# Kernel tuning notes

Hardware: AMD Instinct MI355X
Metric: run time of the kernel (lower is better)

The kernel has to match this reference:

```python
import jax, jax.numpy as jnp
import numpy as np
import math

B, S, D, H = 4, 2048, 768, 12
DK = D // H

def setup_inputs() -> dict:
    key = jax.random.key(0)
    ks = jax.random.split(key, 12)
    sc = 1.0 / math.sqrt(D)
    return {
        'Q': jax.random.normal(ks[0], (B, S, D), jnp.float32),
        'K': jax.random.normal(ks[1], (B, S, D), jnp.float32),
        'V': jax.random.normal(ks[2], (B, S, D), jnp.float32),
        'mask': jax.random.randint(ks[3], (B, 1, S, S), 0, 2, jnp.int32),
        'Wq': jax.random.normal(ks[4], (D, D), jnp.float32) * sc,
        'bq': jnp.zeros((D,), jnp.float32),
        'Wk': jax.random.normal(ks[5], (D, D), jnp.float32) * sc,
        'bk': jnp.zeros((D,), jnp.float32),
        'Wv': jax.random.normal(ks[6], (D, D), jnp.float32) * sc,
        'bv': jnp.zeros((D,), jnp.float32),
        'Wo': jax.random.normal(ks[7], (D, D), jnp.float32) * sc,
        'bo': jnp.zeros((D,), jnp.float32),
    }

def _split_heads(x):
    # [B,S,D] -> [B,H,S,DK]
    return x.reshape(B, S, H, DK).transpose(0, 2, 1, 3)

def reference(Q, K, V, mask, Wq, bq, Wk, bk, Wv, bv, Wo, bo):
    q = _split_heads(Q @ Wq.T + bq)
    k = _split_heads(K @ Wk.T + bk)
    v = _split_heads(V @ Wv.T + bv)
    scores = jnp.einsum('bhqd,bhkd->bhqk', q, k) / math.sqrt(DK)
    # Faithful to the source: masked positions are filled with -1e-9 (NOT -inf)
    scores = jnp.where(mask == 0, jnp.float32(-1e-9), scores)
    attn = jax.nn.softmax(scores, axis=-1)
    x = jnp.einsum('bhqk,bhkd->bhqd', attn, v)          # [B,H,S,DK]
    x = x.transpose(0, 2, 1, 3).reshape(B, S, D)         # [B,S,D]
    return x @ Wo.T + bo
```

## Files before the change

### kernel.cpp

```cpp
#include <hip/hip_runtime.h>

#define BB 4
#define SS 2048
#define DD 768
#define HH 12
#define DKK 64
#define MM (BB*SS)

typedef __attribute__((ext_vector_type(8))) short bf16x8;
typedef __attribute__((ext_vector_type(4))) float f32x4;

#define GLDS(g, l) __builtin_amdgcn_global_load_lds( \
    (const __attribute__((address_space(1))) unsigned int*)(g), \
    (__attribute__((address_space(3))) unsigned int*)(l), 16, 0, 0)

__device__ __forceinline__ unsigned short f2bf(float f) {
    union { float f; unsigned int u; } v; v.f = f;
    unsigned int r = v.u + 0x7fffu + ((v.u >> 16) & 1u);
    return (unsigned short)(r >> 16);
}

#define NACT4 (MM*DD/4)
#define ABLK  (NACT4/256)
#define NW4   (DD*DD/4)
#define WBLK  (NW4/256)
#define MBLK  (BB*SS*SS/256)

__global__ void prep(
    const float* __restrict__ Q, const float* __restrict__ K, const float* __restrict__ V,
    const float* __restrict__ Wq, const float* __restrict__ Wk, const float* __restrict__ Wv,
    const float* __restrict__ Wo, const int* __restrict__ mask,
    unsigned short* __restrict__ Qc, unsigned short* __restrict__ Kc, unsigned short* __restrict__ Vc,
    unsigned short* __restrict__ Wqc, unsigned short* __restrict__ Wkc, unsigned short* __restrict__ Wvc,
    unsigned short* __restrict__ Woc, unsigned int* __restrict__ mbits)
{
    const int bx = blockIdx.x;
    if (bx < 3 * ABLK) {
        const int seg = bx / ABLK;
        const float* s = seg == 0 ? Q : seg == 1 ? K : V;
        unsigned short* d = seg == 0 ? Qc : seg == 1 ? Kc : Vc;
        const int i = (bx - seg * ABLK) * 256 + threadIdx.x;
        float4 v = ((const float4*)s)[i];
        ushort4 o;
        o.x = f2bf(v.x); o.y = f2bf(v.y); o.z = f2bf(v.z); o.w = f2bf(v.w);
        ((ushort4*)d)[i] = o;
    } else if (bx < 3 * ABLK + 4 * WBLK) {
        const int b2 = bx - 3 * ABLK;
        const int seg = b2 / WBLK;
        const float* s = seg == 0 ? Wq : seg == 1 ? Wk : seg == 2 ? Wv : Wo;
        unsigned short* d = seg == 0 ? Wqc : seg == 1 ? Wkc : seg == 2 ? Wvc : Woc;
        const int i = (b2 - seg * WBLK) * 256 + threadIdx.x;
        float4 v = ((const float4*)s)[i];
        ushort4 o;
        o.x = f2bf(v.x); o.y = f2bf(v.y); o.z = f2bf(v.z); o.w = f2bf(v.w);
        ((ushort4*)d)[i] = o;
    } else {
        const int t = (bx - (3 * ABLK + 4 * WBLK)) * 256 + threadIdx.x;
        const int m = mask[t];
        unsigned long long b = __ballot(m != 0);
        const int l = t & 63;
        if (l == 0)       mbits[t >> 5] = (unsigned int)b;
        else if (l == 32) mbits[t >> 5] = (unsigned int)(b >> 32);
    }
}

__global__ __launch_bounds__(256) void gemm_qkv(
    const unsigned short* __restrict__ Qc, const unsigned short* __restrict__ Kc, const unsigned short* __restrict__ Vc,
    const unsigned short* __restrict__ Wq, const unsigned short* __restrict__ Wk, const unsigned short* __restrict__ Wv,
    const float* __restrict__ bq, const float* __restrict__ bk, const float* __restrict__ bv,
    unsigned short* __restrict__ qb, unsigned short* __restrict__ kb, unsigned short* __restrict__ vt)
{
    __shared__ unsigned short As[128*32];
    __shared__ unsigned short Bs[128*32];
    const int mat = blockIdx.z;
    const unsigned short* X = mat == 0 ? Qc : mat == 1 ? Kc : Vc;
    const unsigned short* W = mat == 0 ? Wq : mat == 1 ? Wk : Wv;
    const float* bias        = mat == 0 ? bq : mat == 1 ? bk : bv;

    const int tid  = threadIdx.x;
    const int lane = tid & 63;
    const int w    = tid >> 6;
    const int wm   = w >> 1, wn = w & 1;
    const int quad = lane >> 4, c = lane & 15;
    const int m0 = blockIdx.y * 128, n0 = blockIdx.x * 128;

    f32x4 acc[4][4];
    #pragma unroll
    for (int i = 0; i < 4; i++)
        #pragma unroll
        for (int j = 0; j < 4; j++) acc[i][j] = (f32x4){0.f, 0.f, 0.f, 0.f};

    const int ch0 = tid, ch1 = 256 + tid;
    const int r0 = ch0 >> 2, cc0 = (ch0 & 3) << 3;
    const int r1 = ch1 >> 2, cc1 = (ch1 & 3) << 3;
    const unsigned short* Xg0 = X + (size_t)(m0 + r0) * DD + cc0;
    const unsigned short* Xg1 = X + (size_t)(m0 + r1) * DD + cc1;
    const unsigned short* Wg0 = W + (size_t)(n0 + r0) * DD + cc0;
    const unsigned short* Wg1 = W + (size_t)(n0 + r1) * DD + cc1;

    for (int k0 = 0; k0 < DD; k0 += 32) {
        GLDS(Xg0 + k0, As + ch0 * 8);
        GLDS(Xg1 + k0, As + ch1 * 8);
        GLDS(Wg0 + k0, Bs + ch0 * 8);
        GLDS(Wg1 + k0, Bs + ch1 * 8);
        __syncthreads();
        bf16x8 a[4], b[4];
        #pragma unroll
        for (int t = 0; t < 4; t++) {
            a[t] = *(const bf16x8*)(As + ((wm * 64 + t * 16 + c) * 32 + quad * 8));
            b[t] = *(const bf16x8*)(Bs + ((wn * 64 + t * 16 + c) * 32 + quad * 8));
        }
        #pragma unroll
        for (int tm = 0; tm < 4; tm++)
            #pragma unroll
            for (int tn = 0; tn < 4; tn++)
                acc[tm][tn] = __builtin_amdgcn_mfma_f32_16x16x32_bf16(a[tm], b[tn], acc[tm][tn], 0, 0, 0);
        __syncthreads();
    }

    if (mat < 2) {
        unsigned short* out = mat == 0 ? qb : kb;
        #pragma unroll
        for (int tn = 0; tn < 4; tn++) {
            const int col = n0 + wn * 64 + tn * 16 + c;
            const float bz = bias[col];
            #pragma unroll
            for (int tm = 0; tm < 4; tm++) {
                const int row = m0 + wm * 64 + tm * 16 + quad * 4;
                #pragma unroll
                for (int r = 0; r < 4; r++)
                    out[(size_t)(row + r) * DD + col] = f2bf(acc[tm][tn][r] + bz);
            }
        }
    } else {
        #pragma unroll
        for (int tn = 0; tn < 4; tn++) {
            const int col = n0 + wn * 64 + tn * 16 + c;
            const float bz = bias[col];
            const int h = col >> 6, dk = col & 63;
            #pragma unroll
            for (int tm = 0; tm < 4; tm++) {
                const int row = m0 + wm * 64 + tm * 16 + quad * 4;
                const int bb = row >> 11, s = row & 2047;
                ushort4 pk;
                pk.x = f2bf(acc[tm][tn][0] + bz);
                pk.y = f2bf(acc[tm][tn][1] + bz);
                pk.z = f2bf(acc[tm][tn][2] + bz);
                pk.w = f2bf(acc[tm][tn][3] + bz);
                *(ushort4*)(vt + ((((size_t)bb * HH + h) * DKK + dk) * SS + s)) = pk;
            }
        }
    }
}

#define EXPSCALE 0.18033688011112042f

__global__ __launch_bounds__(256, 3) void flash(
    const unsigned short* __restrict__ qb, const unsigned short* __restrict__ kb,
    const unsigned short* __restrict__ vt, const unsigned int* __restrict__ mbits,
    unsigned short* __restrict__ ob)
{
    __shared__ unsigned short Ks[2][64*64];
    __shared__ unsigned short Vs[2][64*64];

    const int bh = blockIdx.y;
    const int bi = bh / HH, h = bh % HH;
    const int tid  = threadIdx.x;
    const int w    = tid >> 6, lane = tid & 63;
    const int quad = lane >> 4, c = lane & 15;
    const int q0w = blockIdx.x * 128 + w * 32;

    bf16x8 qa[2][2];
    #pragma unroll
    for (int mt = 0; mt < 2; mt++) {
        const unsigned short* qbase = qb + (size_t)(bi * SS + q0w + mt * 16 + c) * DD + h * DKK + quad * 8;
        qa[mt][0] = *(const bf16x8*)(qbase);
        qa[mt][1] = *(const bf16x8*)(qbase + 32);
    }

    const int l0 = tid >> 3, sl = tid & 7;
    const int l1 = 32 + l0;
    const int lc = (sl ^ (l0 & 7)) << 3;
    const int kp0 = ((l0 >> 5) << 5) | (((l0 >> 2) & 3) << 3) | (((l0 >> 4) & 1) << 2) | (l0 & 3);
    const int kp1 = ((l1 >> 5) << 5) | (((l1 >> 2) & 3) << 3) | (((l1 >> 4) & 1) << 2) | (l1 & 3);
    const unsigned short* kg0 = kb + ((size_t)bi * SS + kp0) * DD + h * DKK + lc;
    const unsigned short* kg1 = kb + ((size_t)bi * SS + kp1) * DD + h * DKK + lc;
    const unsigned short* vg0 = vt + (((size_t)bi * HH + h) * DKK + l0) * SS + lc;
    const unsigned short* vg1 = vt + (((size_t)bi * HH + h) * DKK + l1) * SS + lc;

    const unsigned int* mrow0 = mbits + (size_t)(bi * SS + q0w + c) * (SS / 32);
    const unsigned int* mrow1 = mrow0 + (size_t)16 * (SS / 32);

    f32x4 o[2][4];
    #pragma unroll
    for (int mt = 0; mt < 2; mt++)
        #pragma unroll
        for (int dt = 0; dt < 4; dt++) o[mt][dt] = (f32x4){0.f, 0.f, 0.f, 0.f};
    float rs[2] = {0.f, 0.f};

    const int cswz = c & 7;

    GLDS(kg0, Ks[0] + (size_t)tid * 8);
    GLDS(kg1, Ks[0] + (size_t)(256 + tid) * 8);
    GLDS(vg0, Vs[0] + (size_t)tid * 8);
    GLDS(vg1, Vs[0] + (size_t)(256 + tid) * 8);

    for (int t = 0; t < SS / 64; t++) {
        const int k0 = t * 64, par = t & 1;
        __syncthreads();
        if (t < SS / 64 - 1) {
            const size_t ko = (size_t)(k0 + 64);
            GLDS(kg0 + ko * DD, Ks[par ^ 1] + (size_t)tid * 8);
            GLDS(kg1 + ko * DD, Ks[par ^ 1] + (size_t)(256 + tid) * 8);
            GLDS(vg0 + ko,      Vs[par ^ 1] + (size_t)tid * 8);
            GLDS(vg1 + ko,      Vs[par ^ 1] + (size_t)(256 + tid) * 8);
        }

        const uint2 mw0 = *(const uint2*)(mrow0 + (k0 >> 5));
        const uint2 mw1 = *(const uint2*)(mrow1 + (k0 >> 5));
        const unsigned long long mmq[2] = {
            ((((unsigned long long)mw0.y << 32) | mw0.x) >> (quad * 8)),
            ((((unsigned long long)mw1.y << 32) | mw1.x) >> (quad * 8)) };

        #pragma unroll
        for (int p = 0; p < 2; p++) {
            unsigned int pq[2][4];
            #pragma unroll
            for (int tt = 0; tt < 2; tt++) {
                const unsigned short* kbase = &Ks[par][((2 * p + tt) * 16 + c) << 6];
                const bf16x8 kf0 = *(const bf16x8*)(kbase + ((quad ^ cswz) << 3));
                const bf16x8 kf1 = *(const bf16x8*)(kbase + (((4 + quad) ^ cswz) << 3));
                #pragma unroll
                for (int mt = 0; mt < 2; mt++) {
                    f32x4 st = (f32x4){0.f, 0.f, 0.f, 0.f};
                    st = __builtin_amdgcn_mfma_f32_16x16x32_bf16(kf0, qa[mt][0], st, 0, 0, 0);
                    st = __builtin_amdgcn_mfma_f32_16x16x32_bf16(kf1, qa[mt][1], st, 0, 0, 0);
                    const unsigned int mb = (unsigned int)(mmq[mt] >> (p * 32 + tt * 4)) & 15u;
                    #pragma unroll
                    for (int r2 = 0; r2 < 2; r2++) {
                        float sv0 = st[r2 * 2]     * EXPSCALE;
                        float sv1 = st[r2 * 2 + 1] * EXPSCALE;
                        sv0 = (mb & (1u << (r2 * 2)))     ? sv0 : 0.0f;
                        sv1 = (mb & (1u << (r2 * 2 + 1))) ? sv1 : 0.0f;
                        const float p0 = __builtin_amdgcn_exp2f(sv0);
                        const float p1 = __builtin_amdgcn_exp2f(sv1);
                        rs[mt] += p0 + p1;
                        union { float f; unsigned int u; } u0, u1; u0.f = p0; u1.f = p1;
                        pq[mt][tt * 2 + r2] = __builtin_amdgcn_perm(u1.u + 0x8000u, u0.u + 0x8000u, 0x07060302);
                    }
                }
            }
            #pragma unroll
            for (int dt = 0; dt < 4; dt++) {
                const bf16x8 vf = *(const bf16x8*)(&Vs[par][((dt * 16 + c) << 6) + ((((p << 2) + quad) ^ cswz) << 3)]);
                #pragma unroll
                for (int mt = 0; mt < 2; mt++) {
                    union { unsigned int u[4]; bf16x8 v; } pb;
                    pb.u[0] = pq[mt][0]; pb.u[1] = pq[mt][1];
                    pb.u[2] = pq[mt][2]; pb.u[3] = pq[mt][3];
                    o[mt][dt] = __builtin_amdgcn_mfma_f32_16x16x32_bf16(vf, pb.v, o[mt][dt], 0, 0, 0);
                }
            }
        }
    }

    #pragma unroll
    for (int mt = 0; mt < 2; mt++) {
        float v = rs[mt];
        v += __shfl_xor(v, 16);
        v += __shfl_xor(v, 32);
        const float rn = __builtin_amdgcn_rcpf(v);
        unsigned short* op = ob + (size_t)(bi * SS + q0w + mt * 16 + c) * DD + h * DKK + quad * 4;
        #pragma unroll
        for (int dt = 0; dt < 4; dt++) {
            ushort4 pk;
            pk.x = f2bf(o[mt][dt][0] * rn);
            pk.y = f2bf(o[mt][dt][1] * rn);
            pk.z = f2bf(o[mt][dt][2] * rn);
            pk.w = f2bf(o[mt][dt][3] * rn);
            *(ushort4*)(op + dt * 16) = pk;
        }
    }
}

__global__ __launch_bounds__(256) void gemm_out(
    const unsigned short* __restrict__ A, const unsigned short* __restrict__ W,
    const float* __restrict__ bias, float* __restrict__ out)
{
    __shared__ unsigned short As[128*32];
    __shared__ unsigned short Bs[128*32];
    const int tid  = threadIdx.x;
    const int lane = tid & 63;
    const int w    = tid >> 6;
    const int wm   = w >> 1, wn = w & 1;
    const int quad = lane >> 4, c = lane & 15;
    const int m0 = blockIdx.y * 128, n0 = blockIdx.x * 128;

    f32x4 acc[4][4];
    #pragma unroll
    for (int i = 0; i < 4; i++)
        #pragma unroll
        for (int j = 0; j < 4; j++) acc[i][j] = (f32x4){0.f, 0.f, 0.f, 0.f};

    const int ch0 = tid, ch1 = 256 + tid;
    const int r0 = ch0 >> 2, cc0 = (ch0 & 3) << 3;
    const int r1 = ch1 >> 2, cc1 = (ch1 & 3) << 3;
    const unsigned short* Ag0 = A + (size_t)(m0 + r0) * DD + cc0;
    const unsigned short* Ag1 = A + (size_t)(m0 + r1) * DD + cc1;
    const unsigned short* Wg0 = W + (size_t)(n0 + r0) * DD + cc0;
    const unsigned short* Wg1 = W + (size_t)(n0 + r1) * DD + cc1;

    for (int k0 = 0; k0 < DD; k0 += 32) {
        GLDS(Ag0 + k0, As + ch0 * 8);
        GLDS(Ag1 + k0, As + ch1 * 8);
        GLDS(Wg0 + k0, Bs + ch0 * 8);
        GLDS(Wg1 + k0, Bs + ch1 * 8);
        __syncthreads();
        bf16x8 a[4], b[4];
        #pragma unroll
        for (int t = 0; t < 4; t++) {
            a[t] = *(const bf16x8*)(As + ((wm * 64 + t * 16 + c) * 32 + quad * 8));
            b[t] = *(const bf16x8*)(Bs + ((wn * 64 + t * 16 + c) * 32 + quad * 8));
        }
        #pragma unroll
        for (int tm = 0; tm < 4; tm++)
            #pragma unroll
            for (int tn = 0; tn < 4; tn++)
                acc[tm][tn] = __builtin_amdgcn_mfma_f32_16x16x32_bf16(a[tm], b[tn], acc[tm][tn], 0, 0, 0);
        __syncthreads();
    }

    #pragma unroll
    for (int tn = 0; tn < 4; tn++) {
        const int col = n0 + wn * 64 + tn * 16 + c;
        const float bz = bias[col];
        #pragma unroll
        for (int tm = 0; tm < 4; tm++) {
            const int row = m0 + wm * 64 + tm * 16 + quad * 4;
            #pragma unroll
            for (int r = 0; r < 4; r++)
                out[(size_t)(row + r) * DD + col] = acc[tm][tn][r] + bz;
        }
    }
}

extern "C" void kernel_launch(void* const* d_in, const int* in_sizes, int n_in,
                              void* d_out, int out_size, void* d_ws, size_t ws_size,
                              hipStream_t stream) {
    (void)in_sizes; (void)n_in; (void)out_size; (void)ws_size;
    const float* Q    = (const float*)d_in[0];
    const float* K    = (const float*)d_in[1];
    const float* V    = (const float*)d_in[2];
    const int*   mask = (const int*)d_in[3];
    const float* Wq   = (const float*)d_in[4];
    const float* bq   = (const float*)d_in[5];
    const float* Wk   = (const float*)d_in[6];
    const float* bk   = (const float*)d_in[7];
    const float* Wv   = (const float*)d_in[8];
    const float* bv   = (const float*)d_in[9];
    const float* Wo   = (const float*)d_in[10];
    const float* bo   = (const float*)d_in[11];
    float* out = (float*)d_out;

    char* ws = (char*)d_ws;
    size_t off = 0;
    auto alloc = [&](size_t bytes) { char* p = ws + off; off += (bytes + 255) & ~255ULL; return p; };
    const size_t act = (size_t)MM * DD * 2;
    unsigned short* Qc  = (unsigned short*)alloc(act);
    unsigned short* Kc  = (unsigned short*)alloc(act);
    unsigned short* Vc  = (unsigned short*)alloc(act);
    unsigned short* Wqc = (unsigned short*)alloc((size_t)DD * DD * 2);
    unsigned short* Wkc = (unsigned short*)alloc((size_t)DD * DD * 2);
    unsigned short* Wvc = (unsigned short*)alloc((size_t)DD * DD * 2);
    unsigned short* Woc = (unsigned short*)alloc((size_t)DD * DD * 2);
    unsigned short* qb  = (unsigned short*)alloc(act);
    unsigned short* kb  = (unsigned short*)alloc(act);
    unsigned short* vt  = (unsigned short*)alloc(act);
    unsigned int*  mbits = (unsigned int*)alloc((size_t)BB * SS * (SS / 32) * 4);
    unsigned short* ob = Qc;

    prep<<<dim3(3 * ABLK + 4 * WBLK + MBLK), 256, 0, stream>>>(
        Q, K, V, Wq, Wk, Wv, Wo, mask, Qc, Kc, Vc, Wqc, Wkc, Wvc, Woc, mbits);
    gemm_qkv<<<dim3(DD / 128, MM / 128, 3), 256, 0, stream>>>(
        Qc, Kc, Vc, Wqc, Wkc, Wvc, bq, bk, bv, qb, kb, vt);
    flash<<<dim3(SS / 128, BB * HH), 256, 0, stream>>>(qb, kb, vt, mbits, ob);
    gemm_out<<<dim3(DD / 128, MM / 128), 256, 0, stream>>>(ob, Woc, bo, out);
}
```

Baseline: 376.4 us.

## Widen GEMM K-tiles with swizzled LDS, fold softmax scale into Q, MFMA row sums

Both projection GEMMs now stage 64-wide K tiles with an XOR-swizzled LDS layout, which halves the number of barrier rounds and avoids bank conflicts. The exp2 scale factor is folded into the Q projection epilogue, removing a multiply per score in the flash kernel. The flash kernel computes row sums with an extra MFMA against a ones vector instead of scalar adds and cross-lane shuffles, and it prefetches mask words one tile ahead. The costs are doubled LDS use in the GEMMs, extra MFMA work per tile, and row sums taken from bf16-rounded probabilities.

```diff
diff --git a/kernel.cpp b/kernel.cpp
--- a/kernel.cpp
+++ b/kernel.cpp
@@ -19,6 +19,8 @@
     unsigned int r = v.u + 0x7fffu + ((v.u >> 16) & 1u);
     return (unsigned short)(r >> 16);
 }
+
+#define EXPSCALE 0.18033688011112042f
 
 #define NACT4 (MM*DD/4)
 #define ABLK  (NACT4/256)
@@ -70,8 +72,8 @@
     const float* __restrict__ bq, const float* __restrict__ bk, const float* __restrict__ bv,
     unsigned short* __restrict__ qb, unsigned short* __restrict__ kb, unsigned short* __restrict__ vt)
 {
-    __shared__ unsigned short As[128*32];
-    __shared__ unsigned short Bs[128*32];
+    __shared__ unsigned short As[128*64];
+    __shared__ unsigned short Bs[128*64];
     const int mat = blockIdx.z;
     const unsigned short* X = mat == 0 ? Qc : mat == 1 ? Kc : Vc;
     const unsigned short* W = mat == 0 ? Wq : mat == 1 ? Wk : Wv;
@@ -90,36 +92,47 @@
         #pragma unroll
         for (int j = 0; j < 4; j++) acc[i][j] = (f32x4){0.f, 0.f, 0.f, 0.f};
 
-    const int ch0 = tid, ch1 = 256 + tid;
-    const int r0 = ch0 >> 2, cc0 = (ch0 & 3) << 3;
-    const int r1 = ch1 >> 2, cc1 = (ch1 & 3) << 3;
-    const unsigned short* Xg0 = X + (size_t)(m0 + r0) * DD + cc0;
-    const unsigned short* Xg1 = X + (size_t)(m0 + r1) * DD + cc1;
-    const unsigned short* Wg0 = W + (size_t)(n0 + r0) * DD + cc0;
-    const unsigned short* Wg1 = W + (size_t)(n0 + r1) * DD + cc1;
-
-    for (int k0 = 0; k0 < DD; k0 += 32) {
-        GLDS(Xg0 + k0, As + ch0 * 8);
-        GLDS(Xg1 + k0, As + ch1 * 8);
-        GLDS(Wg0 + k0, Bs + ch0 * 8);
-        GLDS(Wg1 + k0, Bs + ch1 * 8);
+    const unsigned short* Xg[4]; const unsigned short* Wg[4]; int dst[4];
+    #pragma unroll
+    for (int j = 0; j < 4; j++) {
+        const int ch = tid + j * 256;
+        const int row = ch >> 3, sl = ch & 7;
+        const int lc = (sl ^ (row & 7)) << 3;
+        Xg[j] = X + (size_t)(m0 + row) * DD + lc;
+        Wg[j] = W + (size_t)(n0 + row) * DD + lc;
+        dst[j] = ch * 8;
+    }
+    const int cswz = c & 7;
+
+    for (int k0 = 0; k0 < DD; k0 += 64) {
+        #pragma unroll
+        for (int j = 0; j < 4; j++) {
+            GLDS(Xg[j] + k0, As + dst[j]);
+            GLDS(Wg[j] + k0, Bs + dst[j]);
+        }
         __syncthreads();
-        bf16x8 a[4], b[4];
-        #pragma unroll
-        for (int t = 0; t < 4; t++) {
-            a[t] = *(const bf16x8*)(As + ((wm * 64 + t * 16 + c) * 32 + quad * 8));
-            b[t] = *(const bf16x8*)(Bs + ((wn * 64 + t * 16 + c) * 32 + quad * 8));
-        }
-        #pragma unroll
-        for (int tm = 0; tm < 4; tm++)
-            #pragma unroll
-            for (int tn = 0; tn < 4; tn++)
-                acc[tm][tn] = __builtin_amdgcn_mfma_f32_16x16x32_bf16(a[tm], b[tn], acc[tm][tn], 0, 0, 0);
+        #pragma unroll
+        for (int kk = 0; kk < 2; kk++) {
+            bf16x8 a[4], b[4];
+            #pragma unroll
+            for (int t = 0; t < 4; t++) {
+                const int ra = wm * 64 + t * 16 + c;
+                const int rb = wn * 64 + t * 16 + c;
+                a[t] = *(const bf16x8*)(As + ra * 64 + (((kk * 4 + quad) ^ cswz) << 3));
+                b[t] = *(const bf16x8*)(Bs + rb * 64 + (((kk * 4 + quad) ^ cswz) << 3));
+            }
+            #pragma unroll
+            for (int tm = 0; tm < 4; tm++)
+                #pragma unroll
+                for (int tn = 0; tn < 4; tn++)
+                    acc[tm][tn] = __builtin_amdgcn_mfma_f32_16x16x32_bf16(a[tm], b[tn], acc[tm][tn], 0, 0, 0);
+        }
         __syncthreads();
     }
 
     if (mat < 2) {
         unsigned short* out = mat == 0 ? qb : kb;
+        const float scale = mat == 0 ? EXPSCALE : 1.0f;
         #pragma unroll
         for (int tn = 0; tn < 4; tn++) {
             const int col = n0 + wn * 64 + tn * 16 + c;
@@ -129,7 +142,7 @@
                 const int row = m0 + wm * 64 + tm * 16 + quad * 4;
                 #pragma unroll
                 for (int r = 0; r < 4; r++)
-                    out[(size_t)(row + r) * DD + col] = f2bf(acc[tm][tn][r] + bz);
+                    out[(size_t)(row + r) * DD + col] = f2bf((acc[tm][tn][r] + bz) * scale);
             }
         }
     } else {
@@ -153,8 +166,6 @@
     }
 }
 
-#define EXPSCALE 0.18033688011112042f
-
 __global__ __launch_bounds__(256, 3) void flash(
     const unsigned short* __restrict__ qb, const unsigned short* __restrict__ kb,
     const unsigned short* __restrict__ vt, const unsigned int* __restrict__ mbits,
@@ -196,7 +207,12 @@
     for (int mt = 0; mt < 2; mt++)
         #pragma unroll
         for (int dt = 0; dt < 4; dt++) o[mt][dt] = (f32x4){0.f, 0.f, 0.f, 0.f};
-    float rs[2] = {0.f, 0.f};
+    f32x4 osum[2] = { (f32x4){0.f,0.f,0.f,0.f}, (f32x4){0.f,0.f,0.f,0.f} };
+    const f32x4 ZC = (f32x4){0.f, 0.f, 0.f, 0.f};
+    union { unsigned int u[4]; bf16x8 v; } onesu;
+    onesu.u[0] = 0x3F803F80u; onesu.u[1] = 0x3F803F80u;
+    onesu.u[2] = 0x3F803F80u; onesu.u[3] = 0x3F803F80u;
+    const bf16x8 ones = onesu.v;
 
     const int cswz = c & 7;
 
@@ -204,20 +220,23 @@
     GLDS(kg1, Ks[0] + (size_t)(256 + tid) * 8);
     GLDS(vg0, Vs[0] + (size_t)tid * 8);
     GLDS(vg1, Vs[0] + (size_t)(256 + tid) * 8);
+    uint2 mw0 = *(const uint2*)(mrow0);
+    uint2 mw1 = *(const uint2*)(mrow1);
 
     for (int t = 0; t < SS / 64; t++) {
         const int k0 = t * 64, par = t & 1;
         __syncthreads();
+        uint2 nw0 = make_uint2(0u, 0u), nw1 = make_uint2(0u, 0u);
         if (t < SS / 64 - 1) {
             const size_t ko = (size_t)(k0 + 64);
             GLDS(kg0 + ko * DD, Ks[par ^ 1] + (size_t)tid * 8);
             GLDS(kg1 + ko * DD, Ks[par ^ 1] + (size_t)(256 + tid) * 8);
             GLDS(vg0 + ko,      Vs[par ^ 1] + (size_t)tid * 8);
             GLDS(vg1 + ko,      Vs[par ^ 1] + (size_t)(256 + tid) * 8);
-        }
-
-        const uint2 mw0 = *(const uint2*)(mrow0 + (k0 >> 5));
-        const uint2 mw1 = *(const uint2*)(mrow1 + (k0 >> 5));
+            nw0 = *(const uint2*)(mrow0 + ((k0 + 64) >> 5));
+            nw1 = *(const uint2*)(mrow1 + ((k0 + 64) >> 5));
+        }
+
         const unsigned long long mmq[2] = {
             ((((unsigned long long)mw0.y << 32) | mw0.x) >> (quad * 8)),
             ((((unsigned long long)mw1.y << 32) | mw1.x) >> (quad * 8)) };
@@ -232,44 +251,43 @@
                 const bf16x8 kf1 = *(const bf16x8*)(kbase + (((4 + quad) ^ cswz) << 3));
                 #pragma unroll
                 for (int mt = 0; mt < 2; mt++) {
-                    f32x4 st = (f32x4){0.f, 0.f, 0.f, 0.f};
-                    st = __builtin_amdgcn_mfma_f32_16x16x32_bf16(kf0, qa[mt][0], st, 0, 0, 0);
+                    f32x4 st = __builtin_amdgcn_mfma_f32_16x16x32_bf16(kf0, qa[mt][0], ZC, 0, 0, 0);
                     st = __builtin_amdgcn_mfma_f32_16x16x32_bf16(kf1, qa[mt][1], st, 0, 0, 0);
                     const unsigned int mb = (unsigned int)(mmq[mt] >> (p * 32 + tt * 4)) & 15u;
                     #pragma unroll
                     for (int r2 = 0; r2 < 2; r2++) {
-                        float sv0 = st[r2 * 2]     * EXPSCALE;
-                        float sv1 = st[r2 * 2 + 1] * EXPSCALE;
-                        sv0 = (mb & (1u << (r2 * 2)))     ? sv0 : 0.0f;
-                        sv1 = (mb & (1u << (r2 * 2 + 1))) ? sv1 : 0.0f;
+                        const float sv0 = (mb & (1u << (r2 * 2)))     ? st[r2 * 2]     : 0.0f;
+                        const float sv1 = (mb & (1u << (r2 * 2 + 1))) ? st[r2 * 2 + 1] : 0.0f;
                         const float p0 = __builtin_amdgcn_exp2f(sv0);
                         const float p1 = __builtin_amdgcn_exp2f(sv1);
-                        rs[mt] += p0 + p1;
                         union { float f; unsigned int u; } u0, u1; u0.f = p0; u1.f = p1;
                         pq[mt][tt * 2 + r2] = __builtin_amdgcn_perm(u1.u + 0x8000u, u0.u + 0x8000u, 0x07060302);
                     }
                 }
             }
+            bf16x8 pbv[2];
+            #pragma unroll
+            for (int mt = 0; mt < 2; mt++) {
+                union { unsigned int u[4]; bf16x8 v; } pb;
+                pb.u[0] = pq[mt][0]; pb.u[1] = pq[mt][1];
+                pb.u[2] = pq[mt][2]; pb.u[3] = pq[mt][3];
+                pbv[mt] = pb.v;
+                osum[mt] = __builtin_amdgcn_mfma_f32_16x16x32_bf16(ones, pbv[mt], osum[mt], 0, 0, 0);
+            }
             #pragma unroll
             for (int dt = 0; dt < 4; dt++) {
                 const bf16x8 vf = *(const bf16x8*)(&Vs[par][((dt * 16 + c) << 6) + ((((p << 2) + quad) ^ cswz) << 3)]);
                 #pragma unroll
-                for (int mt = 0; mt < 2; mt++) {
-                    union { unsigned int u[4]; bf16x8 v; } pb;
-                    pb.u[0] = pq[mt][0]; pb.u[1] = pq[mt][1];
-                    pb.u[2] = pq[mt][2]; pb.u[3] = pq[mt][3];
-                    o[mt][dt] = __builtin_amdgcn_mfma_f32_16x16x32_bf16(vf, pb.v, o[mt][dt], 0, 0, 0);
-                }
-            }
-        }
+                for (int mt = 0; mt < 2; mt++)
+                    o[mt][dt] = __builtin_amdgcn_mfma_f32_16x16x32_bf16(vf, pbv[mt], o[mt][dt], 0, 0, 0);
+            }
+        }
+        mw0 = nw0; mw1 = nw1;
     }
 
     #pragma unroll
     for (int mt = 0; mt < 2; mt++) {
-        float v = rs[mt];
-        v += __shfl_xor(v, 16);
-        v += __shfl_xor(v, 32);
-        const float rn = __builtin_amdgcn_rcpf(v);
+        const float rn = __builtin_amdgcn_rcpf(osum[mt][0]);
         unsigned short* op = ob + (size_t)(bi * SS + q0w + mt * 16 + c) * DD + h * DKK + quad * 4;
         #pragma unroll
         for (int dt = 0; dt < 4; dt++) {
@@ -287,8 +305,8 @@
     const unsigned short* __restrict__ A, const unsigned short* __restrict__ W,
     const float* __restrict__ bias, float* __restrict__ out)
 {
-    __shared__ unsigned short As[128*32];
-    __shared__ unsigned short Bs[128*32];
+    __shared__ unsigned short As[128*64];
+    __shared__ unsigned short Bs[128*64];
     const int tid  = threadIdx.x;
     const int lane = tid & 63;
     const int w    = tid >> 6;
@@ -302,31 +320,41 @@
         #pragma unroll
         for (int j = 0; j < 4; j++) acc[i][j] = (f32x4){0.f, 0.f, 0.f, 0.f};
 
-    const int ch0 = tid, ch1 = 256 + tid;
-    const int r0 = ch0 >> 2, cc0 = (ch0 & 3) << 3;
-    const int r1 = ch1 >> 2, cc1 = (ch1 & 3) << 3;
-    const unsigned short* Ag0 = A + (size_t)(m0 + r0) * DD + cc0;
-    const unsigned short* Ag1 = A + (size_t)(m0 + r1) * DD + cc1;
-    const unsigned short* Wg0 = W + (size_t)(n0 + r0) * DD + cc0;
-    const unsigned short* Wg1 = W + (size_t)(n0 + r1) * DD + cc1;
-
-    for (int k0 = 0; k0 < DD; k0 += 32) {
-        GLDS(Ag0 + k0, As + ch0 * 8);
-        GLDS(Ag1 + k0, As + ch1 * 8);
-        GLDS(Wg0 + k0, Bs + ch0 * 8);
-        GLDS(Wg1 + k0, Bs + ch1 * 8);
+    const unsigned short* Ag[4]; const unsigned short* Wg[4]; int dst[4];
+    #pragma unroll
+    for (int j = 0; j < 4; j++) {
+        const int ch = tid + j * 256;
+        const int row = ch >> 3, sl = ch & 7;
+        const int lcc = (sl ^ (row & 7)) << 3;
+        Ag[j] = A + (size_t)(m0 + row) * DD + lcc;
+        Wg[j] = W + (size_t)(n0 + row) * DD + lcc;
+        dst[j] = ch * 8;
+    }
+    const int cswz = c & 7;
+
+    for (int k0 = 0; k0 < DD; k0 += 64) {
+        #pragma unroll
+        for (int j = 0; j < 4; j++) {
+            GLDS(Ag[j] + k0, As + dst[j]);
+            GLDS(Wg[j] + k0, Bs + dst[j]);
+        }
         __syncthreads();
-        bf16x8 a[4], b[4];
-        #pragma unroll
-        for (int t = 0; t < 4; t++) {
-            a[t] = *(const bf16x8*)(As + ((wm * 64 + t * 16 + c) * 32 + quad * 8));
-            b[t] = *(const bf16x8*)(Bs + ((wn * 64 + t * 16 + c) * 32 + quad * 8));
-        }
-        #pragma unroll
-        for (int tm = 0; tm < 4; tm++)
-            #pragma unroll
-            for (int tn = 0; tn < 4; tn++)
-                acc[tm][tn] = __builtin_amdgcn_mfma_f32_16x16x32_bf16(a[tm], b[tn], acc[tm][tn], 0, 0, 0);
+        #pragma unroll
+        for (int kk = 0; kk < 2; kk++) {
+            bf16x8 a[4], b[4];
+            #pragma unroll
+            for (int t = 0; t < 4; t++) {
+                const int ra = wm * 64 + t * 16 + c;
+                const int rb = wn * 64 + t * 16 + c;
+                a[t] = *(const bf16x8*)(As + ra * 64 + (((kk * 4 + quad) ^ cswz) << 3));
+                b[t] = *(const bf16x8*)(Bs + rb * 64 + (((kk * 4 + quad) ^ cswz) << 3));
+            }
+            #pragma unroll
+            for (int tm = 0; tm < 4; tm++)
+                #pragma unroll
+                for (int tn = 0; tn < 4; tn++)
+                    acc[tm][tn] = __builtin_amdgcn_mfma_f32_16x16x32_bf16(a[tm], b[tn], acc[tm][tn], 0, 0, 0);
+        }
         __syncthreads();
     }
 
```

Result: faster. 357.1 us (-5.1%).
